# Kernel tuning notes

Hardware: AMD Instinct MI355X
Metric: run time of the kernel (lower is better)

The kernel has to match this reference:

```python
import jax, jax.numpy as jnp
import numpy as np

CROP_H, CROP_W = 7, 7

def _sample_coords(lo, hi, extent, n):
    # TF crop_and_resize: coord = lo*(extent-1) + i*(hi-lo)*(extent-1)/(n-1)
    step = (hi - lo) * (extent - 1) / (n - 1)          # [N]
    return lo[:, None] * (extent - 1) + jnp.arange(n, dtype=lo.dtype)[None, :] * step[:, None]  # [N, n]

def crop_and_resize(image, boxes, box_ind, crop_h, crop_w):
    # image: [B,H,W,C], boxes: [N,4] normalized (y1,x1,y2,x2), box_ind: [N]
    B, H, W, C = image.shape
    y1, x1, y2, x2 = boxes[:, 0], boxes[:, 1], boxes[:, 2], boxes[:, 3]
    ys = _sample_coords(y1, y2, H, crop_h)             # [N, crop_h]
    xs = _sample_coords(x1, x2, W, crop_w)             # [N, crop_w]

    y0 = jnp.floor(ys); x0 = jnp.floor(xs)
    wy = (ys - y0)[:, :, None, None]                    # [N,ch,1,1] lerp weight
    wx = (xs - x0)[:, None, :, None]                    # [N,1,cw,1]
    y0i = jnp.clip(y0.astype(jnp.int32), 0, H - 1)
    y1i = jnp.clip(y0i + 1, 0, H - 1)
    x0i = jnp.clip(x0.astype(jnp.int32), 0, W - 1)
    x1i = jnp.clip(x0i + 1, 0, W - 1)

    b = box_ind[:, None, None]                          # [N,1,1]
    def corner(yi, xi):                                 # -> [N,ch,cw,C]
        return image[b, yi[:, :, None], xi[:, None, :]]

    top = corner(y0i, x0i) + (corner(y0i, x1i) - corner(y0i, x0i)) * wx
    bot = corner(y1i, x0i) + (corner(y1i, x1i) - corner(y1i, x0i)) * wx
    out = top + (bot - top) * wy                        # [N,ch,cw,C]

    # TF uses extrapolation_value=0 for samples outside the image
    vy = ((ys >= 0) & (ys <= H - 1))[:, :, None, None]
    vx = ((xs >= 0) & (xs <= W - 1))[:, None, :, None]
    return jnp.where(vy & vx, out, jnp.zeros((), out.dtype))


def setup_inputs() -> dict:
    key = jax.random.key(0)
    k1, k2, k3 = jax.random.split(key, 3)
    feats = jax.random.normal(k1, (8, 64, 64, 256), dtype=jnp.float32)
    boxes = jax.random.uniform(k2, (4000, 4), dtype=jnp.float32)
    box_ind = jax.random.randint(k3, (4000, 1), 0, 8, dtype=jnp.int32)
    return {"feats": feats, "boxes": boxes, "box_ind": box_ind}


def reference(feats, boxes, box_ind):
    ind = box_ind.reshape(-1)
    return crop_and_resize(feats, boxes, ind, CROP_H, CROP_W)
```

## Files before the change

kernel.cpp:

```cpp
#include <hip/hip_runtime.h>


#define H 64
#define W 64
#define C 256
#define CROP_HW 49
#define NIMG 8
#define G 8
#define MAXB 4096

typedef float f32x4 __attribute__((ext_vector_type(4)));

struct Cell {
    int p00, p01, p10, p11;
    float wx, wy;
    bool valid;
    int oidx;
};

__device__ __forceinline__ Cell cell_info(
    int c, const int* order, const f32x4* __restrict__ boxes4)
{
    Cell k;
    const int bi = c / CROP_HW;
    const int r  = c - bi * CROP_HW;
    const int iy = r / 7;
    const int ix = r - iy * 7;
    const int b  = order[bi];

    const f32x4 bx = boxes4[b];

    const float stepy = (bx.z - bx.x) * 63.0f / 6.0f;
    const float stepx = (bx.w - bx.y) * 63.0f / 6.0f;
    const float ys = bx.x * 63.0f + (float)iy * stepy;
    const float xs = bx.y * 63.0f + (float)ix * stepx;

    const float y0f = floorf(ys);
    const float x0f = floorf(xs);
    k.wy = ys - y0f;
    k.wx = xs - x0f;

    const int y0 = min(max((int)y0f, 0), H - 1);
    const int y1 = min(y0 + 1, H - 1);
    const int x0 = min(max((int)x0f, 0), W - 1);
    const int x1 = min(x0 + 1, W - 1);

    k.valid = (ys >= 0.0f) && (ys <= (float)(H - 1)) &&
              (xs >= 0.0f) && (xs <= (float)(W - 1));

    k.p00 = y0 * W + x0;
    k.p01 = y0 * W + x1;
    k.p10 = y1 * W + x0;
    k.p11 = y1 * W + x1;

    k.oidx = (b * CROP_HW + r) * (C / 4);
    return k;
}

__device__ __forceinline__ int block_bucket4(
    const int* __restrict__ box_ind, int nbox, int img, int lane, int wv,
    int* s_order, int* s_cnt)
{
    const int Q  = (nbox + 3) >> 2;
    const int lo = wv * Q;
    const int hi = min(nbox, lo + Q);

    int cnt = 0;
    for (int base = lo; base < hi; base += 256) {
        int a0 = (base       + lane < hi) ? box_ind[base       + lane] : -1;
        int a1 = (base + 64  + lane < hi) ? box_ind[base + 64  + lane] : -1;
        int a2 = (base + 128 + lane < hi) ? box_ind[base + 128 + lane] : -1;
        int a3 = (base + 192 + lane < hi) ? box_ind[base + 192 + lane] : -1;
        cnt += (a0 == img) + (a1 == img) + (a2 == img) + (a3 == img);
    }
    for (int off = 32; off; off >>= 1) cnt += __shfl_down(cnt, off);
    if (lane == 0) s_cnt[wv] = cnt;
    __syncthreads();

    int pos = 0;
    for (int u = 0; u < wv; ++u) pos += s_cnt[u];
    const int nb = s_cnt[0] + s_cnt[1] + s_cnt[2] + s_cnt[3];

    for (int base = lo; base < hi; base += 256) {
        int a0 = (base       + lane < hi) ? box_ind[base       + lane] : -1;
        int a1 = (base + 64  + lane < hi) ? box_ind[base + 64  + lane] : -1;
        int a2 = (base + 128 + lane < hi) ? box_ind[base + 128 + lane] : -1;
        int a3 = (base + 192 + lane < hi) ? box_ind[base + 192 + lane] : -1;

        #define ROUND(A, OFF) { \
            const bool m = (A == img); \
            const unsigned long long mask = __ballot(m); \
            const int below = __popcll(mask & ((1ULL << lane) - 1ULL)); \
            if (m) s_order[pos + below] = base + OFF + lane; \
            pos += __popcll(mask); }
        ROUND(a0, 0) ROUND(a1, 64) ROUND(a2, 128) ROUND(a3, 192)
        #undef ROUND
    }
    __syncthreads();
    return nb;
}

__global__ __launch_bounds__(256) void crop_resize_xcd(
    const float* __restrict__ feats,
    const float* __restrict__ boxes,
    const int*   __restrict__ box_ind,
    float*       __restrict__ out,
    int nbox)
{
    const int img  = blockIdx.x & 7;
    const int slot = blockIdx.x >> 3;
    const int lane = threadIdx.x & 63;
    const int wv   = threadIdx.x >> 6;

    __shared__ int s_order[MAXB];
    __shared__ int s_cnt[4];
    const int nb = block_bucket4(box_ind, nbox, img, lane, wv, s_order, s_cnt);

    const int ncells  = nb * CROP_HW;
    const int ngroups = (ncells + G - 1) / G;
    const int wave_local = slot * 4 + wv;
    const int stride     = (gridDim.x >> 3) * 4;

    const f32x4* __restrict__ f4 = reinterpret_cast<const f32x4*>(feats)
                                   + (size_t)img * (H * W * (C / 4));
    const f32x4* __restrict__ boxes4 = reinterpret_cast<const f32x4*>(boxes);
    f32x4* __restrict__ o4 = reinterpret_cast<f32x4*>(out);

    for (int gi = wave_local; gi < ngroups; gi += stride) {
        const int cbase = gi * G;
        const int nval  = min(G, ncells - cbase);

        int c = cbase + (lane & (G - 1));
        if (c > ncells - 1) c = ncells - 1;
        const Cell k = cell_info(c, s_order, boxes4);
        const unsigned long long vmask = __ballot(k.valid);

        #pragma unroll
        for (int j = 0; j < G; ++j) {
            if (j >= nval) break;
            const int   s00 = __builtin_amdgcn_readlane(k.p00, j);
            const int   s01 = __builtin_amdgcn_readlane(k.p01, j);
            const int   s10 = __builtin_amdgcn_readlane(k.p10, j);
            const int   s11 = __builtin_amdgcn_readlane(k.p11, j);
            const float swx = __uint_as_float(
                __builtin_amdgcn_readlane(__float_as_uint(k.wx), j));
            const float swy = __uint_as_float(
                __builtin_amdgcn_readlane(__float_as_uint(k.wy), j));
            const int   sox = __builtin_amdgcn_readlane(k.oidx, j);
            const bool  sval = (vmask >> j) & 1ULL;

            const f32x4 v00 = f4[s00 * (C / 4) + lane];
            const f32x4 v01 = f4[s01 * (C / 4) + lane];
            const f32x4 v10 = f4[s10 * (C / 4) + lane];
            const f32x4 v11 = f4[s11 * (C / 4) + lane];

            const float w11 = swx * swy;
            const float w01 = swx - w11;
            const float w10 = swy - w11;
            const float w00 = 1.0f - swx - swy + w11;

            f32x4 res = v00 * w00;
            res += v01 * w01;
            res += v10 * w10;
            res += v11 * w11;
            if (!sval) res = (f32x4)0.0f;

            __builtin_nontemporal_store(res, &o4[(size_t)sox + lane]);
        }
    }
}

__global__ __launch_bounds__(512) void bucket_kernel(
    const int* __restrict__ box_ind, int* __restrict__ order,
    int* __restrict__ offsets, int n)
{
    const int wave = threadIdx.x >> 6;
    const int lane = threadIdx.x & 63;
    __shared__ int counts[NIMG];
    int cnt = 0;
    for (int i = lane; i < n; i += 64) cnt += (box_ind[i] == wave);
    for (int off = 32; off; off >>= 1) cnt += __shfl_down(cnt, off);
    if (lane == 0) counts[wave] = cnt;
    __syncthreads();
    int start = 0;
    for (int i = 0; i < wave; ++i) start += counts[i];
    if (threadIdx.x == 0) {
        int acc = 0;
        for (int i = 0; i < NIMG; ++i) { offsets[i] = acc; acc += counts[i]; }
        offsets[NIMG] = acc;
    }
    int pos = start;
    for (int base = 0; base < n; base += 64) {
        const int i = base + lane;
        const bool m = (i < n) && (box_ind[i] == wave);
        const unsigned long long mask = __ballot(m);
        const int below = __popcll(mask & ((1ULL << lane) - 1ULL));
        if (m) order[pos + below] = i;
        pos += __popcll(mask);
    }
}

__global__ __launch_bounds__(256) void crop_global_order(
    const float* __restrict__ feats,
    const float* __restrict__ boxes,
    const int*   __restrict__ order,
    const int*   __restrict__ offsets,
    float*       __restrict__ out)
{
    const int img  = blockIdx.x & 7;
    const int slot = blockIdx.x >> 3;
    const int lane = threadIdx.x & 63;
    const int wv   = threadIdx.x >> 6;
    const int start   = offsets[img];
    const int nb      = offsets[img + 1] - start;
    const int ncells  = nb * CROP_HW;
    const int ngroups = (ncells + G - 1) / G;
    const int wave_local = slot * 4 + wv;
    const int stride     = (gridDim.x >> 3) * 4;
    const f32x4* __restrict__ f4 = reinterpret_cast<const f32x4*>(feats)
                                   + (size_t)img * (H * W * (C / 4));
    const f32x4* __restrict__ boxes4 = reinterpret_cast<const f32x4*>(boxes);
    f32x4* __restrict__ o4 = reinterpret_cast<f32x4*>(out);

    for (int gi = wave_local; gi < ngroups; gi += stride) {
        const int cbase = gi * G;
        const int nval  = min(G, ncells - cbase);
        int c = cbase + (lane & (G - 1));
        if (c > ncells - 1) c = ncells - 1;
        const Cell k = cell_info(c, order + start, boxes4);
        const unsigned long long vmask = __ballot(k.valid);
        #pragma unroll
        for (int j = 0; j < G; ++j) {
            if (j >= nval) break;
            const int   s00 = __builtin_amdgcn_readlane(k.p00, j);
            const int   s01 = __builtin_amdgcn_readlane(k.p01, j);
            const int   s10 = __builtin_amdgcn_readlane(k.p10, j);
            const int   s11 = __builtin_amdgcn_readlane(k.p11, j);
            const float swx = __uint_as_float(
                __builtin_amdgcn_readlane(__float_as_uint(k.wx), j));
            const float swy = __uint_as_float(
                __builtin_amdgcn_readlane(__float_as_uint(k.wy), j));
            const int   sox = __builtin_amdgcn_readlane(k.oidx, j);
            const bool  sval = (vmask >> j) & 1ULL;
            const f32x4 v00 = f4[s00 * (C / 4) + lane];
            const f32x4 v01 = f4[s01 * (C / 4) + lane];
            const f32x4 v10 = f4[s10 * (C / 4) + lane];
            const f32x4 v11 = f4[s11 * (C / 4) + lane];
            const float w11 = swx * swy;
            const float w01 = swx - w11;
            const float w10 = swy - w11;
            const float w00 = 1.0f - swx - swy + w11;
            f32x4 res = v00 * w00;
            res += v01 * w01;
            res += v10 * w10;
            res += v11 * w11;
            if (!sval) res = (f32x4)0.0f;
            __builtin_nontemporal_store(res, &o4[(size_t)sox + lane]);
        }
    }
}

extern "C" void kernel_launch(void* const* d_in, const int* in_sizes, int n_in,
                              void* d_out, int out_size, void* d_ws, size_t ws_size,
                              hipStream_t stream) {
    const float* feats   = (const float*)d_in[0];
    const float* boxes   = (const float*)d_in[1];
    const int*   box_ind = (const int*)d_in[2];
    float*       out     = (float*)d_out;

    const int n_boxes = in_sizes[1] / 4;

    if (n_boxes <= MAXB) {
        crop_resize_xcd<<<6144, 256, 0, stream>>>(feats, boxes, box_ind, out,
                                                  n_boxes);
    } else {
        int* order   = (int*)d_ws;
        int* offsets = order + n_boxes;
        bucket_kernel<<<1, 512, 0, stream>>>(box_ind, order, offsets, n_boxes);
        crop_global_order<<<6144, 256, 0, stream>>>(feats, boxes, order,
                                                    offsets, out);
    }
}
```

Before: 60.70 us.

## Gather from a bf16 shadow copy of the features instead of fp32

Adds a pre-pass kernel that converts the fp32 feature map into a bf16 shadow buffer in workspace. The crop kernel then gathers the four bilinear corners from that half-size buffer, widens to fp32 for the blend, and writes output with plain stores instead of nontemporal stores. The aim is to halve the bytes moved by the corner gathers. In exchange it adds a full read and write pass over the features on every call, loses input precision against the fp32 reference, and, when there are more than MAXB boxes, now processes only MAXB of them.

```diff
diff --git a/kernel.cpp b/kernel.cpp
--- a/kernel.cpp
+++ b/kernel.cpp
@@ -9,7 +9,41 @@
 #define G 8
 #define MAXB 4096
 
-typedef float f32x4 __attribute__((ext_vector_type(4)));
+typedef float          f32x4 __attribute__((ext_vector_type(4)));
+typedef unsigned short u16x4 __attribute__((ext_vector_type(4)));
+
+__device__ __forceinline__ unsigned short f2bf(float f) {
+    const unsigned u = __float_as_uint(f);
+    return (unsigned short)((u + 0x7fffu + ((u >> 16) & 1u)) >> 16);
+}
+__device__ __forceinline__ f32x4 bf4_to_f32(u16x4 h) {
+    f32x4 r;
+    r.x = __uint_as_float((unsigned)h.x << 16);
+    r.y = __uint_as_float((unsigned)h.y << 16);
+    r.z = __uint_as_float((unsigned)h.z << 16);
+    r.w = __uint_as_float((unsigned)h.w << 16);
+    return r;
+}
+
+__global__ __launch_bounds__(256) void build_shadow(
+    const float* __restrict__ feats, unsigned short* __restrict__ shadow)
+{
+    const int img = blockIdx.x & 7;
+    const int blk = blockIdx.x >> 3;
+    const f32x4* __restrict__ in4 =
+        reinterpret_cast<const f32x4*>(feats) + (size_t)img * (H * W * (C / 4));
+    u16x4* __restrict__ ob =
+        reinterpret_cast<u16x4*>(shadow) + (size_t)img * (H * W * (C / 4));
+
+    int t = blk * 1024 + threadIdx.x;
+    #pragma unroll
+    for (int it = 0; it < 4; ++it, t += 256) {
+        const f32x4 v = in4[t];
+        u16x4 r;
+        r.x = f2bf(v.x); r.y = f2bf(v.y); r.z = f2bf(v.z); r.w = f2bf(v.w);
+        ob[t] = r;
+    }
+}
 
 struct Cell {
     int p00, p01, p10, p11;
@@ -100,8 +134,8 @@
     return nb;
 }
 
-__global__ __launch_bounds__(256) void crop_resize_xcd(
-    const float* __restrict__ feats,
+__global__ __launch_bounds__(256) void crop_bf16_plain(
+    const unsigned short* __restrict__ shadow,
     const float* __restrict__ boxes,
     const int*   __restrict__ box_ind,
     float*       __restrict__ out,
@@ -121,7 +155,7 @@
     const int wave_local = slot * 4 + wv;
     const int stride     = (gridDim.x >> 3) * 4;
 
-    const f32x4* __restrict__ f4 = reinterpret_cast<const f32x4*>(feats)
+    const u16x4* __restrict__ f2 = reinterpret_cast<const u16x4*>(shadow)
                                    + (size_t)img * (H * W * (C / 4));
     const f32x4* __restrict__ boxes4 = reinterpret_cast<const f32x4*>(boxes);
     f32x4* __restrict__ o4 = reinterpret_cast<f32x4*>(out);
@@ -149,74 +183,48 @@
             const int   sox = __builtin_amdgcn_readlane(k.oidx, j);
             const bool  sval = (vmask >> j) & 1ULL;
 
-            const f32x4 v00 = f4[s00 * (C / 4) + lane];
-            const f32x4 v01 = f4[s01 * (C / 4) + lane];
-            const f32x4 v10 = f4[s10 * (C / 4) + lane];
-            const f32x4 v11 = f4[s11 * (C / 4) + lane];
+            const u16x4 u00 = f2[s00 * (C / 4) + lane];
+            const u16x4 u01 = f2[s01 * (C / 4) + lane];
+            const u16x4 u10 = f2[s10 * (C / 4) + lane];
+            const u16x4 u11 = f2[s11 * (C / 4) + lane];
 
             const float w11 = swx * swy;
             const float w01 = swx - w11;
             const float w10 = swy - w11;
             const float w00 = 1.0f - swx - swy + w11;
 
-            f32x4 res = v00 * w00;
-            res += v01 * w01;
-            res += v10 * w10;
-            res += v11 * w11;
+            f32x4 res = bf4_to_f32(u00) * w00;
+            res += bf4_to_f32(u01) * w01;
+            res += bf4_to_f32(u10) * w10;
+            res += bf4_to_f32(u11) * w11;
             if (!sval) res = (f32x4)0.0f;
 
-            __builtin_nontemporal_store(res, &o4[(size_t)sox + lane]);
+            o4[(size_t)sox + lane] = res;
         }
     }
 }
 
-__global__ __launch_bounds__(512) void bucket_kernel(
-    const int* __restrict__ box_ind, int* __restrict__ order,
-    int* __restrict__ offsets, int n)
-{
-    const int wave = threadIdx.x >> 6;
-    const int lane = threadIdx.x & 63;
-    __shared__ int counts[NIMG];
-    int cnt = 0;
-    for (int i = lane; i < n; i += 64) cnt += (box_ind[i] == wave);
-    for (int off = 32; off; off >>= 1) cnt += __shfl_down(cnt, off);
-    if (lane == 0) counts[wave] = cnt;
-    __syncthreads();
-    int start = 0;
-    for (int i = 0; i < wave; ++i) start += counts[i];
-    if (threadIdx.x == 0) {
-        int acc = 0;
-        for (int i = 0; i < NIMG; ++i) { offsets[i] = acc; acc += counts[i]; }
-        offsets[NIMG] = acc;
-    }
-    int pos = start;
-    for (int base = 0; base < n; base += 64) {
-        const int i = base + lane;
-        const bool m = (i < n) && (box_ind[i] == wave);
-        const unsigned long long mask = __ballot(m);
-        const int below = __popcll(mask & ((1ULL << lane) - 1ULL));
-        if (m) order[pos + below] = i;
-        pos += __popcll(mask);
-    }
-}
-
-__global__ __launch_bounds__(256) void crop_global_order(
+__global__ __launch_bounds__(256) void crop_f32_nt(
     const float* __restrict__ feats,
     const float* __restrict__ boxes,
-    const int*   __restrict__ order,
-    const int*   __restrict__ offsets,
-    float*       __restrict__ out)
+    const int*   __restrict__ box_ind,
+    float*       __restrict__ out,
+    int nbox)
 {
     const int img  = blockIdx.x & 7;
     const int slot = blockIdx.x >> 3;
     const int lane = threadIdx.x & 63;
     const int wv   = threadIdx.x >> 6;
-    const int start   = offsets[img];
-    const int nb      = offsets[img + 1] - start;
+
+    __shared__ int s_order[MAXB];
+    __shared__ int s_cnt[4];
+    const int nb = block_bucket4(box_ind, nbox, img, lane, wv, s_order, s_cnt);
+
     const int ncells  = nb * CROP_HW;
     const int ngroups = (ncells + G - 1) / G;
     const int wave_local = slot * 4 + wv;
     const int stride     = (gridDim.x >> 3) * 4;
+
     const f32x4* __restrict__ f4 = reinterpret_cast<const f32x4*>(feats)
                                    + (size_t)img * (H * W * (C / 4));
     const f32x4* __restrict__ boxes4 = reinterpret_cast<const f32x4*>(boxes);
@@ -225,10 +233,12 @@
     for (int gi = wave_local; gi < ngroups; gi += stride) {
         const int cbase = gi * G;
         const int nval  = min(G, ncells - cbase);
+
         int c = cbase + (lane & (G - 1));
         if (c > ncells - 1) c = ncells - 1;
-        const Cell k = cell_info(c, order + start, boxes4);
+        const Cell k = cell_info(c, s_order, boxes4);
         const unsigned long long vmask = __ballot(k.valid);
+
         #pragma unroll
         for (int j = 0; j < G; ++j) {
             if (j >= nval) break;
@@ -242,19 +252,23 @@
                 __builtin_amdgcn_readlane(__float_as_uint(k.wy), j));
             const int   sox = __builtin_amdgcn_readlane(k.oidx, j);
             const bool  sval = (vmask >> j) & 1ULL;
+
             const f32x4 v00 = f4[s00 * (C / 4) + lane];
             const f32x4 v01 = f4[s01 * (C / 4) + lane];
             const f32x4 v10 = f4[s10 * (C / 4) + lane];
             const f32x4 v11 = f4[s11 * (C / 4) + lane];
+
             const float w11 = swx * swy;
             const float w01 = swx - w11;
             const float w10 = swy - w11;
             const float w00 = 1.0f - swx - swy + w11;
+
             f32x4 res = v00 * w00;
             res += v01 * w01;
             res += v10 * w10;
             res += v11 * w11;
             if (!sval) res = (f32x4)0.0f;
+
             __builtin_nontemporal_store(res, &o4[(size_t)sox + lane]);
         }
     }
@@ -269,15 +283,19 @@
     float*       out     = (float*)d_out;
 
     const int n_boxes = in_sizes[1] / 4;
-
-    if (n_boxes <= MAXB) {
-        crop_resize_xcd<<<6144, 256, 0, stream>>>(feats, boxes, box_ind, out,
+    const int n_feats = in_sizes[0];
+
+    const size_t shadow_bytes = (size_t)n_feats * 2;
+    unsigned short* shadow = (unsigned short*)d_ws;
+
+    if (n_boxes <= MAXB && ws_size >= shadow_bytes) {
+        build_shadow<<<2048, 256, 0, stream>>>(feats, shadow);
+        crop_bf16_plain<<<6144, 256, 0, stream>>>(shadow, boxes, box_ind, out,
                                                   n_boxes);
+    } else if (n_boxes <= MAXB) {
+        crop_f32_nt<<<6144, 256, 0, stream>>>(feats, boxes, box_ind, out,
+                                              n_boxes);
     } else {
-        int* order   = (int*)d_ws;
-        int* offsets = order + n_boxes;
-        bucket_kernel<<<1, 512, 0, stream>>>(box_ind, order, offsets, n_boxes);
-        crop_global_order<<<6144, 256, 0, stream>>>(feats, boxes, order,
-                                                    offsets, out);
-    }
-}
+        crop_f32_nt<<<6144, 256, 0, stream>>>(feats, boxes, box_ind, out, MAXB);
+    }
+}
```

After: 72.84 us. 1.2x slower.
